# Performance work log

Measured on AMD Instinct MI355X. Metric: run time of the kernel, lower is better.

Reference implementation:

```python
import jax, jax.numpy as jnp
import numpy as np

P, B, A, NBT, NC, NTAB, G = 512, 512, 32, 40, 3, 40, 36
NA = B * A


def setup_inputs() -> dict:
    key = jax.random.key(0)
    rng = np.random.default_rng(0)
    coords = jax.random.normal(key, (P, NA, 3), dtype=jnp.float32) * 3.0
    # residue b occupies atoms [b*A, (b+1)*A)
    offsets = np.broadcast_to(np.arange(B, dtype=np.int32) * A, (P, B)).copy()
    block_type = rng.integers(0, NBT, size=(P, B)).astype(np.int32)
    # simple linear chain per pose: conn 0 = lower (prev residue), conn 1 = upper (next residue)
    inter = np.full((P, B, NC, 2), -1, dtype=np.int32)
    inter[:, 1:, 0, 0] = np.arange(B - 1, dtype=np.int32)
    inter[:, 1:, 0, 1] = 1
    inter[:, :-1, 1, 0] = np.arange(1, B, dtype=np.int32)
    inter[:, :-1, 1, 1] = 0
    down = rng.integers(0, A, size=(NBT, NC, A)).astype(np.int32)
    bt_rama_table = rng.integers(0, NTAB, size=(NBT, 2)).astype(np.int32)
    bt_upper_conn_ind = np.ones(NBT, dtype=np.int32)
    bt_is_pro = rng.integers(0, 2, size=NBT).astype(np.int32)
    # unresolved torsion atoms: (local_atom_ind, conn_ind, n_bonds_from_conn); atom_ind<0 => via connection
    tor = np.zeros((NBT, 8, 3), dtype=np.int32)
    tor[:, 0] = (-1, 0, 0)  # phi: prev-C via lower conn
    tor[:, 1] = (0, -1, 0)  # N
    tor[:, 2] = (1, -1, 0)  # CA
    tor[:, 3] = (2, -1, 0)  # C
    tor[:, 4] = (0, -1, 0)  # psi: N
    tor[:, 5] = (1, -1, 0)  # CA
    tor[:, 6] = (2, -1, 0)  # C
    tor[:, 7] = (-1, 1, 0)  # next-N via upper conn
    rama_tables = jax.random.normal(jax.random.fold_in(key, 1), (NTAB, G, G), dtype=jnp.float32)
    tp = np.zeros((NTAB, 2, 2), dtype=np.float32)
    tp[:, 0, :] = -np.pi            # bb start
    tp[:, 1, :] = 2.0 * np.pi / G   # bb step
    return dict(
        coords=coords,
        pose_stack_block_coord_offset=jnp.asarray(offsets),
        pose_stack_block_type=jnp.asarray(block_type),
        pose_stack_inter_residue_connections=jnp.asarray(inter),
        bt_atom_downstream_of_conn=jnp.asarray(down),
        bt_rama_table=jnp.asarray(bt_rama_table),
        bt_upper_conn_ind=jnp.asarray(bt_upper_conn_ind),
        bt_is_pro=jnp.asarray(bt_is_pro),
        bt_rama_torsion_atoms=jnp.asarray(tor),
        rama_tables=rama_tables,
        table_params=jnp.asarray(tp),
    )


def _dihedral(p):
    # p: [..., 4, 3] -> dihedral angle [...] via atan2 formulation
    b1 = p[..., 1, :] - p[..., 0, :]
    b2 = p[..., 2, :] - p[..., 1, :]
    b3 = p[..., 3, :] - p[..., 2, :]
    n1 = jnp.cross(b1, b2)
    n2 = jnp.cross(b2, b3)
    b2n = b2 / (jnp.linalg.norm(b2, axis=-1, keepdims=True) + 1e-12)
    m1 = jnp.cross(n1, b2n)
    x = jnp.sum(n1 * n2, axis=-1)
    y = jnp.sum(m1 * n2, axis=-1)
    return jnp.arctan2(y, x)


def _catmull_rom_w(f):
    # weights over 4 neighbors (i-1, i, i+1, i+2); f in [0,1)
    f2 = f * f
    f3 = f2 * f
    return jnp.stack(
        [0.5 * (-f3 + 2 * f2 - f), 0.5 * (3 * f3 - 5 * f2 + 2),
         0.5 * (-3 * f3 + 4 * f2 + f), 0.5 * (f3 - f2)], axis=-1)


def reference(coords, pose_stack_block_coord_offset, pose_stack_block_type,
              pose_stack_inter_residue_connections, bt_atom_downstream_of_conn,
              bt_rama_table, bt_upper_conn_ind, bt_is_pro, bt_rama_torsion_atoms,
              rama_tables, table_params):
    nP, nB = pose_stack_block_type.shape
    nG = rama_tables.shape[-1]
    pidx = jnp.arange(nP)[:, None, None]
    bidx = jnp.arange(nB)[None, :, None]
    bt = pose_stack_block_type                       # [P,B]
    tor = bt_rama_torsion_atoms[bt]                  # [P,B,8,3]
    atom_ind, conn_ind, nbonds = tor[..., 0], tor[..., 1], tor[..., 2]
    safe_conn = jnp.clip(conn_ind, 0, None)
    other_block = pose_stack_inter_residue_connections[pidx, bidx, safe_conn, 0]  # [P,B,8]
    other_conn = pose_stack_inter_residue_connections[pidx, bidx, safe_conn, 1]
    conn_ok = (conn_ind >= 0) & (other_block >= 0)
    ob = jnp.clip(other_block, 0, None)
    oc = jnp.clip(other_conn, 0, None)
    obt = bt[pidx, ob]                               # [P,B,8]
    down_atom = bt_atom_downstream_of_conn[obt, oc, nbonds]
    conn_global = pose_stack_block_coord_offset[pidx, ob] + down_atom
    local_global = pose_stack_block_coord_offset[pidx, bidx] + jnp.clip(atom_ind, 0, None)
    use_local = atom_ind >= 0
    gidx = jnp.where(use_local, local_global, conn_global)  # [P,B,8]
    atom_ok = use_local | conn_ok
    xyz = coords[pidx, gidx]                         # [P,B,8,3]
    ang = _dihedral(xyz.reshape(nP, nB, 2, 4, 3))    # [P,B,2] -> (phi, psi)
    tor_ok = jnp.all(atom_ok.reshape(nP, nB, 2, 4), axis=-1)
    # table selection: proline-dependent on the NEXT residue
    uc = bt_upper_conn_ind[bt]                       # [P,B]
    p2 = jnp.arange(nP)[:, None]
    b2 = jnp.arange(nB)[None, :]
    nb = pose_stack_inter_residue_connections[p2, b2, uc, 0]  # [P,B]
    nb_ok = nb >= 0
    nbt = bt[p2, jnp.clip(nb, 0, None)]
    tab = bt_rama_table[bt, bt_is_pro[nbt]]          # [P,B]
    start = table_params[tab, 0]                     # [P,B,2]
    step = table_params[tab, 1]
    u = (ang - start) / step                         # [P,B,2]
    i0f = jnp.floor(u)
    f = u - i0f
    i0 = i0f.astype(jnp.int32)
    offs = jnp.arange(-1, 3, dtype=jnp.int32)        # 4 spline neighbors
    ii = jnp.mod(i0[..., 0:1] + offs, nG)            # [P,B,4] periodic phi bins
    jj = jnp.mod(i0[..., 1:2] + offs, nG)            # [P,B,4] periodic psi bins
    wphi = _catmull_rom_w(f[..., 0])                 # [P,B,4]
    wpsi = _catmull_rom_w(f[..., 1])
    vals = rama_tables[tab[..., None, None], ii[..., :, None], jj[..., None, :]]  # [P,B,4,4]
    e = jnp.einsum('pbi,pbj,pbij->pb', wphi, wpsi, vals)
    ok = tor_ok[..., 0] & tor_ok[..., 1] & nb_ok
    return jnp.sum(jnp.where(ok, e, 0.0), axis=-1)   # [P] per-pose rama score
```

## Files before the change

kernel.cpp:

```cpp
#include <hip/hip_runtime.h>
#include <math.h>

#define NP 512
#define NBLK 512
#define NA_ 32
#define NCn 3
#define NG 36

struct F3 { float x, y, z; };
__device__ inline F3 f3sub(F3 a, F3 b) { return {a.x - b.x, a.y - b.y, a.z - b.z}; }
__device__ inline F3 f3cross(F3 a, F3 b) {
    return {a.y * b.z - a.z * b.y, a.z * b.x - a.x * b.z, a.x * b.y - a.y * b.x};
}
__device__ inline float f3dot(F3 a, F3 b) { return a.x * b.x + a.y * b.y + a.z * b.z; }

__global__ __launch_bounds__(NBLK) void rama_kernel(
    const float* __restrict__ coords,
    const int*   __restrict__ offsets,
    const int*   __restrict__ block_type,
    const int*   __restrict__ inter,
    const int*   __restrict__ down,
    const int*   __restrict__ bt_rama_table,
    const int*   __restrict__ bt_upper_conn,
    const int*   __restrict__ bt_is_pro,
    const int*   __restrict__ tor_atoms,
    const float* __restrict__ rama_tables,
    const float* __restrict__ table_params,
    float*       __restrict__ out)
{
    const int p  = blockIdx.x;
    const int b  = threadIdx.x;
    const int pb = p * NBLK + b;

    const int bt    = block_type[pb];
    const int off_b = offsets[pb];
    const float* pose_coords = coords + (size_t)p * NBLK * NA_ * 3;

    float ang[2];
    bool  tok[2];
    #pragma unroll
    for (int t = 0; t < 2; ++t) {
        F3 pts[4];
        bool ok4 = true;
        #pragma unroll
        for (int a = 0; a < 4; ++a) {
            const int ti       = (bt * 8 + t * 4 + a) * 3;
            const int atom_ind = tor_atoms[ti + 0];
            const int conn_ind = tor_atoms[ti + 1];
            const int nbonds   = tor_atoms[ti + 2];
            int g;
            if (atom_ind >= 0) {
                g = off_b + atom_ind;
            } else {
                const int sc = conn_ind > 0 ? conn_ind : 0;
                const int ib = (pb * NCn + sc) * 2;
                const int ob = inter[ib + 0];
                const int oc = inter[ib + 1];
                ok4 = ok4 && (conn_ind >= 0) && (ob >= 0);
                const int obc = ob > 0 ? ob : 0;
                const int occ = oc > 0 ? oc : 0;
                const int obt = block_type[p * NBLK + obc];
                const int da  = down[(obt * NCn + occ) * NA_ + nbonds];
                g = offsets[p * NBLK + obc] + da;
            }
            const float* c = pose_coords + (size_t)g * 3;
            pts[a] = {c[0], c[1], c[2]};
        }
        const F3 b1 = f3sub(pts[1], pts[0]);
        const F3 b2 = f3sub(pts[2], pts[1]);
        const F3 b3 = f3sub(pts[3], pts[2]);
        const F3 n1 = f3cross(b1, b2);
        const F3 n2 = f3cross(b2, b3);
        const float inv = 1.0f / (sqrtf(f3dot(b2, b2)) + 1e-12f);
        const F3 b2n = {b2.x * inv, b2.y * inv, b2.z * inv};
        const F3 m1  = f3cross(n1, b2n);
        ang[t] = atan2f(f3dot(m1, n2), f3dot(n1, n2));
        tok[t] = ok4;
    }

    const int uc    = bt_upper_conn[bt];
    const int nb    = inter[(pb * NCn + uc) * 2 + 0];
    const bool nbok = nb >= 0;
    const int nbc   = nb > 0 ? nb : 0;
    const int nbt_  = block_type[p * NBLK + nbc];
    const int tab   = bt_rama_table[bt * 2 + bt_is_pro[nbt_]];

    float e = 0.0f;
    if (tok[0] && tok[1] && nbok) {
        float w0[4], w1[4];
        int   ii[4], jj[4];
        #pragma unroll
        for (int d = 0; d < 2; ++d) {
            const float start = table_params[(tab * 2 + 0) * 2 + d];
            const float step  = table_params[(tab * 2 + 1) * 2 + d];
            const float u   = (ang[d] - start) / step;
            const float i0f = floorf(u);
            const float f   = u - i0f;
            const int   i0  = (int)i0f;
            const float f2 = f * f, f3 = f2 * f;
            float* w = (d == 0) ? w0 : w1;
            w[0] = 0.5f * (-f3 + 2.0f * f2 - f);
            w[1] = 0.5f * (3.0f * f3 - 5.0f * f2 + 2.0f);
            w[2] = 0.5f * (-3.0f * f3 + 4.0f * f2 + f);
            w[3] = 0.5f * (f3 - f2);
            int* idx = (d == 0) ? ii : jj;
            #pragma unroll
            for (int k = 0; k < 4; ++k) {
                int v = (i0 - 1 + k) % NG;
                if (v < 0) v += NG;
                idx[k] = v;
            }
        }
        const float* T = rama_tables + (size_t)tab * NG * NG;
        #pragma unroll
        for (int i = 0; i < 4; ++i) {
            const float* Tr = T + ii[i] * NG;
            float rowsum = 0.0f;
            #pragma unroll
            for (int j = 0; j < 4; ++j) rowsum += w1[j] * Tr[jj[j]];
            e += w0[i] * rowsum;
        }
    }

    float v = e;
    #pragma unroll
    for (int o = 32; o > 0; o >>= 1) v += __shfl_down(v, o);
    __shared__ float partial[NBLK / 64];
    const int wave = threadIdx.x >> 6;
    const int lane = threadIdx.x & 63;
    if (lane == 0) partial[wave] = v;
    __syncthreads();
    if (threadIdx.x == 0) {
        float s = 0.0f;
        #pragma unroll
        for (int i = 0; i < NBLK / 64; ++i) s += partial[i];
        out[p] = s;
    }
}

extern "C" void kernel_launch(void* const* d_in, const int* in_sizes, int n_in,
                              void* d_out, int out_size, void* d_ws, size_t ws_size,
                              hipStream_t stream) {
    (void)in_sizes; (void)n_in; (void)out_size; (void)d_ws; (void)ws_size;
    rama_kernel<<<NP, NBLK, 0, stream>>>(
        (const float*)d_in[0],
        (const int*)d_in[1],
        (const int*)d_in[2],
        (const int*)d_in[3],
        (const int*)d_in[4],
        (const int*)d_in[5],
        (const int*)d_in[6],
        (const int*)d_in[7],
        (const int*)d_in[8],
        (const float*)d_in[9],
        (const float*)d_in[10],
        (float*)d_out);
}
```

Before: 176.9 us.

## Stage per-pose and per-type lookup tables in LDS and batch all coordinate gathers

Each block now cooperatively copies the pose's block types, offsets and connections, plus the small per-type tables (torsion atoms, downstream atoms, rama table ids, table params), into shared memory. All eight atom indices are resolved from LDS before any coordinate is loaded, so the eight coordinate gathers can be issued together instead of as dependent chains of global loads. This trades extra LDS usage and a barrier, with some loads of whole tables every block, for less global-memory latency on the indirect index chain.

```diff
diff --git a/kernel.cpp b/kernel.cpp
--- a/kernel.cpp
+++ b/kernel.cpp
@@ -6,6 +6,8 @@
 #define NA_ 32
 #define NCn 3
 #define NG 36
+#define NBT 40
+#define NTAB 40
 
 struct F3 { float x, y, z; };
 __device__ inline F3 f3sub(F3 a, F3 b) { return {a.x - b.x, a.y - b.y, a.z - b.z}; }
@@ -28,81 +30,109 @@
     const float* __restrict__ table_params,
     float*       __restrict__ out)
 {
-    const int p  = blockIdx.x;
-    const int b  = threadIdx.x;
-    const int pb = p * NBLK + b;
+    __shared__ int   s_bt[NBLK];
+    __shared__ int   s_off[NBLK];
+    __shared__ int   s_inter[NBLK * NCn * 2];
+    __shared__ int   s_tor[NBT * 8 * 3];
+    __shared__ int   s_down[NBT * NCn * NA_];
+    __shared__ int   s_rt[NBT * 2];
+    __shared__ int   s_uc[NBT];
+    __shared__ int   s_pro[NBT];
+    __shared__ float s_tp[NTAB * 4];
+    __shared__ float partial[NBLK / 64];
 
-    const int bt    = block_type[pb];
-    const int off_b = offsets[pb];
+    const int p   = blockIdx.x;
+    const int tid = threadIdx.x;
+
+    s_bt[tid]  = block_type[p * NBLK + tid];
+    s_off[tid] = offsets[p * NBLK + tid];
+    #pragma unroll
+    for (int i = tid; i < NBLK * NCn * 2; i += NBLK)
+        s_inter[i] = inter[p * NBLK * NCn * 2 + i];
+    for (int i = tid; i < NBT * 24; i += NBLK)  s_tor[i]  = tor_atoms[i];
+    for (int i = tid; i < NBT * NCn * NA_; i += NBLK) s_down[i] = down[i];
+    if (tid < NBT * 2)  s_rt[tid]  = bt_rama_table[tid];
+    if (tid < NBT)      { s_uc[tid] = bt_upper_conn[tid]; s_pro[tid] = bt_is_pro[tid]; }
+    if (tid < NTAB * 4) s_tp[tid]  = table_params[tid];
+    __syncthreads();
+
+    const int b     = tid;
+    const int bt    = s_bt[b];
+    const int off_b = s_off[b];
     const float* pose_coords = coords + (size_t)p * NBLK * NA_ * 3;
 
+    int  g[8];
+    bool ok[8];
+    #pragma unroll
+    for (int k = 0; k < 8; ++k) {
+        const int ti       = (bt * 8 + k) * 3;
+        const int atom_ind = s_tor[ti + 0];
+        const int conn_ind = s_tor[ti + 1];
+        const int nbonds   = s_tor[ti + 2];
+        if (atom_ind >= 0) {
+            g[k]  = off_b + atom_ind;
+            ok[k] = true;
+        } else {
+            const int sc  = conn_ind > 0 ? conn_ind : 0;
+            const int ib  = (b * NCn + sc) * 2;
+            const int ob  = s_inter[ib + 0];
+            const int oc  = s_inter[ib + 1];
+            ok[k] = (conn_ind >= 0) && (ob >= 0);
+            const int obc = ob > 0 ? ob : 0;
+            const int occ = oc > 0 ? oc : 0;
+            const int obt = s_bt[obc];
+            g[k] = s_off[obc] + s_down[(obt * NCn + occ) * NA_ + nbonds];
+        }
+    }
+
+    const int uc    = s_uc[bt];
+    const int nb    = s_inter[(b * NCn + uc) * 2 + 0];
+    const bool nbok = nb >= 0;
+    const int nbc   = nb > 0 ? nb : 0;
+    const int tab   = s_rt[bt * 2 + s_pro[s_bt[nbc]]];
+
+    F3 pts[8];
+    #pragma unroll
+    for (int k = 0; k < 8; ++k) {
+        const float* c = pose_coords + (size_t)g[k] * 3;
+        pts[k] = {c[0], c[1], c[2]};
+    }
+
     float ang[2];
-    bool  tok[2];
     #pragma unroll
     for (int t = 0; t < 2; ++t) {
-        F3 pts[4];
-        bool ok4 = true;
-        #pragma unroll
-        for (int a = 0; a < 4; ++a) {
-            const int ti       = (bt * 8 + t * 4 + a) * 3;
-            const int atom_ind = tor_atoms[ti + 0];
-            const int conn_ind = tor_atoms[ti + 1];
-            const int nbonds   = tor_atoms[ti + 2];
-            int g;
-            if (atom_ind >= 0) {
-                g = off_b + atom_ind;
-            } else {
-                const int sc = conn_ind > 0 ? conn_ind : 0;
-                const int ib = (pb * NCn + sc) * 2;
-                const int ob = inter[ib + 0];
-                const int oc = inter[ib + 1];
-                ok4 = ok4 && (conn_ind >= 0) && (ob >= 0);
-                const int obc = ob > 0 ? ob : 0;
-                const int occ = oc > 0 ? oc : 0;
-                const int obt = block_type[p * NBLK + obc];
-                const int da  = down[(obt * NCn + occ) * NA_ + nbonds];
-                g = offsets[p * NBLK + obc] + da;
-            }
-            const float* c = pose_coords + (size_t)g * 3;
-            pts[a] = {c[0], c[1], c[2]};
-        }
-        const F3 b1 = f3sub(pts[1], pts[0]);
-        const F3 b2 = f3sub(pts[2], pts[1]);
-        const F3 b3 = f3sub(pts[3], pts[2]);
+        const F3* q = pts + t * 4;
+        const F3 b1 = f3sub(q[1], q[0]);
+        const F3 b2 = f3sub(q[2], q[1]);
+        const F3 b3 = f3sub(q[3], q[2]);
         const F3 n1 = f3cross(b1, b2);
         const F3 n2 = f3cross(b2, b3);
         const float inv = 1.0f / (sqrtf(f3dot(b2, b2)) + 1e-12f);
         const F3 b2n = {b2.x * inv, b2.y * inv, b2.z * inv};
         const F3 m1  = f3cross(n1, b2n);
         ang[t] = atan2f(f3dot(m1, n2), f3dot(n1, n2));
-        tok[t] = ok4;
     }
 
-    const int uc    = bt_upper_conn[bt];
-    const int nb    = inter[(pb * NCn + uc) * 2 + 0];
-    const bool nbok = nb >= 0;
-    const int nbc   = nb > 0 ? nb : 0;
-    const int nbt_  = block_type[p * NBLK + nbc];
-    const int tab   = bt_rama_table[bt * 2 + bt_is_pro[nbt_]];
+    const bool all_ok = ok[0] & ok[1] & ok[2] & ok[3] & ok[4] & ok[5] & ok[6] & ok[7] & nbok;
 
     float e = 0.0f;
-    if (tok[0] && tok[1] && nbok) {
+    if (all_ok) {
         float w0[4], w1[4];
         int   ii[4], jj[4];
         #pragma unroll
         for (int d = 0; d < 2; ++d) {
-            const float start = table_params[(tab * 2 + 0) * 2 + d];
-            const float step  = table_params[(tab * 2 + 1) * 2 + d];
+            const float start = s_tp[tab * 4 + d];
+            const float step  = s_tp[tab * 4 + 2 + d];
             const float u   = (ang[d] - start) / step;
             const float i0f = floorf(u);
             const float f   = u - i0f;
             const int   i0  = (int)i0f;
-            const float f2 = f * f, f3 = f2 * f;
+            const float f2 = f * f, f3v = f2 * f;
             float* w = (d == 0) ? w0 : w1;
-            w[0] = 0.5f * (-f3 + 2.0f * f2 - f);
-            w[1] = 0.5f * (3.0f * f3 - 5.0f * f2 + 2.0f);
-            w[2] = 0.5f * (-3.0f * f3 + 4.0f * f2 + f);
-            w[3] = 0.5f * (f3 - f2);
+            w[0] = 0.5f * (-f3v + 2.0f * f2 - f);
+            w[1] = 0.5f * (3.0f * f3v - 5.0f * f2 + 2.0f);
+            w[2] = 0.5f * (-3.0f * f3v + 4.0f * f2 + f);
+            w[3] = 0.5f * (f3v - f2);
             int* idx = (d == 0) ? ii : jj;
             #pragma unroll
             for (int k = 0; k < 4; ++k) {
@@ -125,12 +155,11 @@
     float v = e;
     #pragma unroll
     for (int o = 32; o > 0; o >>= 1) v += __shfl_down(v, o);
-    __shared__ float partial[NBLK / 64];
-    const int wave = threadIdx.x >> 6;
-    const int lane = threadIdx.x & 63;
+    const int wave = tid >> 6;
+    const int lane = tid & 63;
     if (lane == 0) partial[wave] = v;
     __syncthreads();
-    if (threadIdx.x == 0) {
+    if (tid == 0) {
         float s = 0.0f;
         #pragma unroll
         for (int i = 0; i < NBLK / 64; ++i) s += partial[i];
```

Result: faster. 173.2 us (-2.1%).
